# Optimization experiments

Measured on AMD Instinct MI355X. Metric: run time of the kernel, lower is better.

Reference implementation:

```python
import jax, jax.numpy as jnp
import numpy as np

EPS_LN = 1e-12
EPS_BN = 1e-5


def layernorm(x, w, b):
    u = jnp.mean(x, axis=-1, keepdims=True)
    s = jnp.mean((x - u) ** 2, axis=-1, keepdims=True)
    return w * ((x - u) / jnp.sqrt(s + EPS_LN)) + b


def reps_block(x, ln1_w, ln1_b, lin_w, lin_b, ln2_w, ln2_b):
    # GRAPHLayerNorm -> (dropout, identity in eval) -> Linear -> ReLU -> GRAPHLayerNorm
    h = layernorm(x, ln1_w, ln1_b)
    h = jax.nn.relu(jnp.einsum('bnd,od->bno', h, lin_w) + lin_b)
    return layernorm(h, ln2_w, ln2_b)


def attend(x):
    # full dense self-attention: softmax(x x^T) x ; dropout is identity in eval
    scores = jnp.einsum('bnd,bmd->bnm', x, x)  # [B,4096,4096]
    attn = jax.nn.softmax(scores, axis=-1)
    return jnp.einsum('bnm,bmd->bnd', attn, x)


def setup_inputs() -> dict:
    key = jax.random.key(0)
    ks = jax.random.split(key, 8)
    B, C, H, W = 4, 512, 64, 64
    D = 512
    inp = {
        'T1': jax.random.normal(ks[0], (B, C, H, W), jnp.float32),
        'T2': jax.random.normal(ks[1], (B, C, H, W), jnp.float32),
        'w_conv3': jax.random.normal(ks[2], (1024, 1024, 3, 3), jnp.float32) * 0.01,
        'w_conv1': jax.random.normal(ks[3], (512, 1024, 1, 1), jnp.float32) * 0.03,
        'bn_gamma': jnp.ones((512,), jnp.float32),
        'bn_beta': jnp.zeros((512,), jnp.float32),
        'bn_mean': jnp.zeros((512,), jnp.float32),
        'bn_var': jnp.ones((512,), jnp.float32),
        'ln1_w': jnp.ones((D,), jnp.float32),
        'ln1_b': jnp.zeros((D,), jnp.float32),
        'lin_w': jax.random.normal(ks[4], (D, D), jnp.float32) * 0.04,
        'lin_b': jnp.zeros((D,), jnp.float32),
        'ln2_w': jnp.ones((D,), jnp.float32),
        'ln2_b': jnp.zeros((D,), jnp.float32),
    }
    return inp


def reference(T1, T2, w_conv3, w_conv1, bn_gamma, bn_beta, bn_mean, bn_var,
              ln1_w, ln1_b, lin_w, lin_b, ln2_w, ln2_b):
    B = T1.shape[0]
    X = jnp.concatenate((T1, T2), axis=1)  # [B,1024,64,64]
    dn = ('NCHW', 'OIHW', 'NCHW')
    X = jax.lax.conv_general_dilated(X, w_conv3, (1, 1), ((1, 1), (1, 1)), dimension_numbers=dn)
    X = jax.lax.conv_general_dilated(X, w_conv1, (1, 1), ((0, 0), (0, 0)), dimension_numbers=dn)  # [B,512,64,64]
    # BatchNorm (eval, running stats) + ReLU
    inv = (bn_gamma / jnp.sqrt(bn_var + EPS_BN))[None, :, None, None]
    X = jax.nn.relu(X * inv + (bn_beta - bn_mean * bn_gamma / jnp.sqrt(bn_var + EPS_BN))[None, :, None, None])
    x = X.transpose(0, 2, 3, 1).reshape(B, 4096, 512)
    # block 1
    rel = attend(x)
    rel = reps_block(x + rel, ln1_w, ln1_b, lin_w, lin_b, ln2_w, ln2_b)
    # block 2 (original code reuses self.reps_graph, i.e. SAME params)
    rel1 = attend(rel)
    rel1 = reps_block(rel + rel1, ln1_w, ln1_b, lin_w, lin_b, ln2_w, ln2_b)
    return rel1.reshape(B, 64, 64, 512).transpose(0, 3, 1, 2)  # [B,512,64,64]
```

## Files before the change

kernel.cpp:

```cpp
#include <hip/hip_runtime.h>
#include <stdint.h>

typedef float f32x4 __attribute__((ext_vector_type(4)));
typedef __bf16 bf16x8 __attribute__((ext_vector_type(8)));
typedef unsigned short u16;
typedef unsigned short u16x8 __attribute__((ext_vector_type(8)));

__device__ __forceinline__ float bf2f(u16 u){ unsigned int i = ((unsigned int)u)<<16; float f; __builtin_memcpy(&f,&i,4); return f; }
__device__ __forceinline__ u16 f2bf(float f){ unsigned int i; __builtin_memcpy(&i,&f,4); i += 0x7FFFu + ((i>>16)&1u); return (u16)(i>>16); }
__device__ __forceinline__ u16 f2h(float f){ _Float16 h = (_Float16)f; u16 b; __builtin_memcpy(&b,&h,2); return b; }
__device__ __forceinline__ float h2f(u16 b){ _Float16 h; __builtin_memcpy(&h,&b,2); return (float)h; }

__device__ __forceinline__ void gld16(const void* g, void* l){
  __builtin_amdgcn_global_load_lds(
      (const __attribute__((address_space(1))) void*)(uintptr_t)g,
      (__attribute__((address_space(3))) void*)(unsigned int)(uintptr_t)l, 16, 0, 0);
}

__global__ __launch_bounds__(256) void pad_interior(const float* __restrict__ T1,
                                                    const float* __restrict__ T2,
                                                    u16* __restrict__ Xpad){
  const int n = blockIdx.z, ct = blockIdx.y, pt = blockIdx.x;
  const int t = threadIdx.x;
  const int c0 = ct*64, p0 = pt*64;
  const float* src = (c0 < 512) ? (T1 + ((long)n*512 + c0)*4096)
                                : (T2 + ((long)n*512 + (c0-512))*4096);
  __shared__ u16 lds[64][66];
  #pragma unroll
  for (int i=0;i<4;i++){
    int c = i*16 + (t>>4);
    int ch = t&15;
    float4 v = *(const float4*)(src + (long)c*4096 + p0 + ch*4);
    int p = ch*4;
    lds[p+0][c] = f2bf(v.x); lds[p+1][c] = f2bf(v.y);
    lds[p+2][c] = f2bf(v.z); lds[p+3][c] = f2bf(v.w);
  }
  __syncthreads();
  #pragma unroll
  for (int i=0;i<8;i++){
    int p = i*8 + (t>>5);
    int c2 = t&31;
    int pix = p0 + p; int yy = (pix>>6)+1, xx = (pix&63)+1;
    ushort2 val; val.x = lds[p][2*c2]; val.y = lds[p][2*c2+1];
    *(ushort2*)(Xpad + (((long)n*66 + yy)*66 + xx)*1024 + c0 + 2*c2) = val;
  }
}

__global__ __launch_bounds__(256) void prep_w3(const float* __restrict__ w3, u16* __restrict__ wk3t){
  const int o = blockIdx.x; const int t = threadIdx.x;
  __shared__ u16 lds[9216];
  const float* src = w3 + (long)o*9216;
  #pragma unroll
  for (int i=0;i<9;i++){
    int j = i*256 + t;
    float4 v = *(const float4*)(src + j*4);
    lds[j*4+0]=f2bf(v.x); lds[j*4+1]=f2bf(v.y); lds[j*4+2]=f2bf(v.z); lds[j*4+3]=f2bf(v.w);
  }
  __syncthreads();
  u16* dst = wk3t + (long)o*9216;
  #pragma unroll
  for (int i=0;i<36;i++){
    int j = i*256 + t; int tp = j>>10, ci = j&1023;
    dst[j] = lds[ci*9+tp];
  }
}

__global__ void prep_w1(const float* __restrict__ w1, const float* __restrict__ bg,
                        const float* __restrict__ bv, u16* __restrict__ w1t){
  long i = (long)blockIdx.x*256 + threadIdx.x;
  int o = (int)(i>>10);
  float inv = bg[o] / sqrtf(bv[o] + 1e-5f);
  w1t[i] = f2bf(w1[i]*inv);
}

__global__ void prep_bias1(const float* __restrict__ bg, const float* __restrict__ bb,
                           const float* __restrict__ bm, const float* __restrict__ bv,
                           float* __restrict__ bias1){
  int o = blockIdx.x*256+threadIdx.x;
  float inv = bg[o]/sqrtf(bv[o]+1e-5f);
  bias1[o] = bb[o] - bm[o]*inv;
}

__global__ void cvt_bf(const float* __restrict__ s, u16* __restrict__ d){
  long i = (long)blockIdx.x*256 + threadIdx.x;
  d[i] = f2bf(s[i]);
}

__global__ __launch_bounds__(256) void row_norm(const u16* __restrict__ x, float* __restrict__ nrm){
  const int row = blockIdx.x*4 + (threadIdx.x>>6);
  const int lane = threadIdx.x & 63;
  u16x8 q = *(const u16x8*)(x + (long)row*512 + lane*8);
  float s = 0.f;
  #pragma unroll
  for (int j=0;j<8;j++){ float f = bf2f(q[j]); s += f*f; }
  #pragma unroll
  for (int off=32; off; off>>=1) s += __shfl_xor(s, off);
  if (lane==0) nrm[row] = s;
}

__global__ __launch_bounds__(256) void transpose_bf(const u16* __restrict__ src, u16* __restrict__ dst,
                                                    int R, int C, long sStr, long dStr){
  const int z = blockIdx.z;
  src += (long)z*sStr; dst += (long)z*dStr;
  const int r0 = blockIdx.x*64, c0 = blockIdx.y*64;
  const int t = threadIdx.x;
  __shared__ u16 lds[64][66];
  #pragma unroll
  for (int i=0;i<4;i++){
    int r = i*16 + (t>>4), ch = t&15;
    ushort4 v = *(const ushort4*)(src + (long)(r0+r)*C + c0 + ch*4);
    lds[r][ch*4+0]=v.x; lds[r][ch*4+1]=v.y; lds[r][ch*4+2]=v.z; lds[r][ch*4+3]=v.w;
  }
  __syncthreads();
  #pragma unroll
  for (int i=0;i<4;i++){
    int c = i*16 + (t>>4), ch = t&15;
    ushort4 v;
    v.x = lds[ch*4+0][c]; v.y = lds[ch*4+1][c]; v.z = lds[ch*4+2][c]; v.w = lds[ch*4+3][c];
    *(ushort4*)(dst + (long)(c0+c)*R + r0 + ch*4) = v;
  }
}

__global__ __launch_bounds__(256) void transpose_f32(const float* __restrict__ src, float* __restrict__ dst,
                                                     int R, int C, long sStr, long dStr){
  const int z = blockIdx.z;
  src += (long)z*sStr; dst += (long)z*dStr;
  const int r0 = blockIdx.x*32, c0 = blockIdx.y*32;
  const int t = threadIdx.x;
  __shared__ float lds[32][33];
  {
    int r = t>>3, ch = t&7;
    float4 v = *(const float4*)(src + (long)(r0+r)*C + c0 + ch*4);
    lds[r][ch*4+0]=v.x; lds[r][ch*4+1]=v.y; lds[r][ch*4+2]=v.z; lds[r][ch*4+3]=v.w;
  }
  __syncthreads();
  {
    int c = t>>3, ch = t&7;
    float4 v;
    v.x = lds[ch*4+0][c]; v.y = lds[ch*4+1][c]; v.z = lds[ch*4+2][c]; v.w = lds[ch*4+3][c];
    *(float4*)(dst + (long)(c0+c)*R + r0 + ch*4) = v;
  }
}

template<int EPI, int CONV>
__global__ __launch_bounds__(512, 2) void gemm256(
    const u16* __restrict__ A, const u16* __restrict__ Bt, void* __restrict__ Cv,
    int K, int lda, int ldb, int ldc, const float* __restrict__ srow)
{
  extern __shared__ u16 sm[];
  const int t = threadIdx.x;
  const int lane = t & 63;
  const int wid = t >> 6;
  const int wr = wid >> 2, wc = wid & 3;

  const int orig = blockIdx.y * gridDim.x + blockIdx.x;
  const int cpx = (gridDim.x * gridDim.y) >> 3;
  const int swz = (orig & 7) * cpx + (orig >> 3);
  const int bx = swz % gridDim.x;
  const int by = swz / gridDim.x;
  const long m0 = (long)by * 256, n0 = (long)bx * 256;

  const int row0 = t >> 2;
  const int cs0  = (t & 3) ^ ((row0 >> 1) & 3);

  const u16 *aB0, *aB1;
  if (CONV) {
    long m_ = m0 + row0;
    long pb0 = ((long)((int)(m_>>12)*66 + (int)((m_>>6)&63)))*66 + (int)(m_&63);
    m_ = m0 + row0 + 128;
    long pb1 = ((long)((int)(m_>>12)*66 + (int)((m_>>6)&63)))*66 + (int)(m_&63);
    aB0 = A + pb0*1024 + cs0*8;
    aB1 = A + pb1*1024 + cs0*8;
  } else {
    aB0 = A + (m0 + row0)*(long)lda + cs0*8;
    aB1 = A + (m0 + row0 + 128)*(long)lda + cs0*8;
  }
  const u16* bB0 = Bt + (n0 + row0)*(long)ldb + cs0*8;
  const u16* bB1 = Bt + (n0 + row0 + 128)*(long)ldb + cs0*8;

  auto issueA = [&](int sub, long aoff){
    u16* d = sm + sub*8192 + t*8;
    gld16(aB0 + aoff, d);
    gld16(aB1 + aoff, d + 4096);
  };
  auto issueB = [&](int sub, long boff){
    u16* d = sm + 32768 + sub*8192 + t*8;
    gld16(bB0 + boff, d);
    gld16(bB1 + boff, d + 4096);
  };
  auto conv_aoff = [&](int tile)->long {
    int kb = tile << 6;
    int tap = kb >> 10;
    int cb  = kb & 1023;
    int ky = (tap >= 6) ? 2 : (tap >= 3 ? 1 : 0);
    int kx = tap - ky*3;
    return (long)(ky*66 + kx)*1024 + cb;
  };

  const int frow = lane & 15;
  const int elemoff = (((lane>>4) ^ ((frow>>1)&3)) << 3);
  const int rAoff = (wr*128 + frow)*32 + elemoff;
  const int rBoff = (wc*64  + frow)*32 + elemoff;

  f32x4 acc[8][4] = {};

  {
    long a0 = CONV ? conv_aoff(0) : 0L;
    issueA(0, a0);
    issueB(0, 0);
    issueA(1, a0 + 32);
    issueB(1, 32);
  }

  const int NT = K >> 6;
  for (int tile = 0; tile < NT; ++tile) {
    const int b = tile & 1;
    const int nb2 = b ^ 1;
    const bool lastT = (tile == NT-1);
    long aoffN = 0, boffN = 0;
    if (!lastT) {
      aoffN = CONV ? conv_aoff(tile+1) : (long)(tile+1)*64;
      boffN = (long)(tile+1)*64;
    }

    asm volatile("s_waitcnt vmcnt(4)" ::: "memory");
    __builtin_amdgcn_s_barrier();
    __builtin_amdgcn_sched_barrier(0);

    {
      const u16* pA = sm + (b*2+0)*8192 + rAoff;
      const u16* pB = sm + 32768 + (b*2+0)*8192 + rBoff;
      bf16x8 bf[4];
      #pragma unroll
      for (int i=0;i<4;i++) bf[i] = *(const bf16x8*)(pB + i*512);
      {
        bf16x8 a[4];
        #pragma unroll
        for (int i=0;i<4;i++) a[i] = *(const bf16x8*)(pA + i*512);
        if (!lastT) issueA(nb2*2+0, aoffN);
        __builtin_amdgcn_s_setprio(1);
        #pragma unroll
        for (int mi=0;mi<4;mi++)
          #pragma unroll
          for (int ni=0;ni<4;ni++)
            acc[mi][ni] = __builtin_amdgcn_mfma_f32_16x16x32_bf16(a[mi], bf[ni], acc[mi][ni],0,0,0);
        __builtin_amdgcn_s_setprio(0);
      }
      {
        bf16x8 a[4];
        #pragma unroll
        for (int i=0;i<4;i++) a[i] = *(const bf16x8*)(pA + (4+i)*512);
        if (!lastT) issueB(nb2*2+0, boffN);
        __builtin_amdgcn_s_setprio(1);
        #pragma unroll
        for (int mi=0;mi<4;mi++)
          #pragma unroll
          for (int ni=0;ni<4;ni++)
            acc[4+mi][ni] = __builtin_amdgcn_mfma_f32_16x16x32_bf16(a[mi], bf[ni], acc[4+mi][ni],0,0,0);
        __builtin_amdgcn_s_setprio(0);
      }
    }

    if (lastT) asm volatile("s_waitcnt vmcnt(0)" ::: "memory");
    else       asm volatile("s_waitcnt vmcnt(4)" ::: "memory");
    __builtin_amdgcn_s_barrier();
    __builtin_amdgcn_sched_barrier(0);

    {
      const u16* pA = sm + (b*2+1)*8192 + rAoff;
      const u16* pB = sm + 32768 + (b*2+1)*8192 + rBoff;
      bf16x8 bf[4];
      #pragma unroll
      for (int i=0;i<4;i++) bf[i] = *(const bf16x8*)(pB + i*512);
      {
        bf16x8 a[4];
        #pragma unroll
        for (int i=0;i<4;i++) a[i] = *(const bf16x8*)(pA + i*512);
        if (!lastT) issueA(nb2*2+1, aoffN + 32);
        __builtin_amdgcn_s_setprio(1);
        #pragma unroll
        for (int mi=0;mi<4;mi++)
          #pragma unroll
          for (int ni=0;ni<4;ni++)
            acc[mi][ni] = __builtin_amdgcn_mfma_f32_16x16x32_bf16(a[mi], bf[ni], acc[mi][ni],0,0,0);
        __builtin_amdgcn_s_setprio(0);
      }
      {
        bf16x8 a[4];
        #pragma unroll
        for (int i=0;i<4;i++) a[i] = *(const bf16x8*)(pA + (4+i)*512);
        if (!lastT) issueB(nb2*2+1, boffN + 32);
        __builtin_amdgcn_s_setprio(1);
        #pragma unroll
        for (int mi=0;mi<4;mi++)
          #pragma unroll
          for (int ni=0;ni<4;ni++)
            acc[4+mi][ni] = __builtin_amdgcn_mfma_f32_16x16x32_bf16(a[mi], bf[ni], acc[4+mi][ni],0,0,0);
        __builtin_amdgcn_s_setprio(0);
      }
    }
  }

  const int crow0 = wr*128 + ((lane>>4)<<2);
  const int ccol0 = wc*64 + frow;
  #pragma unroll
  for (int mi=0;mi<8;mi++){
    #pragma unroll
    for (int ni=0;ni<4;ni++){
      long col = n0 + ccol0 + ni*16;
      #pragma unroll
      for (int r=0;r<4;r++){
        long row = m0 + crow0 + mi*16 + r;
        float v = acc[mi][ni][r];
        if (EPI==3) ((u16*)Cv)[row*(long)ldc + col] = f2h(v - srow[row]);
        else        ((u16*)Cv)[row*(long)ldc + col] = f2bf(v);
      }
    }
  }
}

template<int EPI>
__global__ __launch_bounds__(256, 2) void gemm_bt(
    const u16* __restrict__ A, const u16* __restrict__ Bt,
    void* __restrict__ Cv, const float* __restrict__ bias,
    int K, int lda, int ldb, int ldc)
{
  const int t = threadIdx.x;
  const int lane = t & 63;
  const int w = t >> 6;
  const int wr = w >> 1, wc = w & 1;
  const long m0 = (long)blockIdx.y * 128;
  const long n0 = (long)blockIdx.x * 128;

  __shared__ u16 lA[128*32];
  __shared__ u16 lB[128*32];

  const u16* aS0 = A + (m0 + (t>>2))*(long)lda + (t&3)*8;
  const u16* aS1 = aS0 + 64*(long)lda;
  const u16* bS0 = Bt + (n0 + (t>>2))*(long)ldb + (t&3)*8;
  const u16* bS1 = bS0 + 64*(long)ldb;
  u16* dA0 = lA + t*8; u16* dA1 = lA + 2048 + t*8;
  u16* dB0 = lB + t*8; u16* dB1 = lB + 2048 + t*8;

  f32x4 acc[4][4] = {};
  const int frow = lane & 15, kq = (lane >> 4) * 8;
  const u16* rA = lA + (wr*64 + frow)*32 + kq;
  const u16* rB = lB + (wc*64 + frow)*32 + kq;

  for (int kb = 0; kb < K; kb += 32) {
    gld16(aS0 + kb, dA0); gld16(aS1 + kb, dA1);
    gld16(bS0 + kb, dB0); gld16(bS1 + kb, dB1);
    __syncthreads();
    bf16x8 af[4], bfr[4];
    #pragma unroll
    for (int i=0;i<4;i++) af[i]  = *(const bf16x8*)(rA + i*512);
    #pragma unroll
    for (int i=0;i<4;i++) bfr[i] = *(const bf16x8*)(rB + i*512);
    #pragma unroll
    for (int mi=0;mi<4;mi++)
      #pragma unroll
      for (int ni=0;ni<4;ni++)
        acc[mi][ni] = __builtin_amdgcn_mfma_f32_16x16x32_bf16(af[mi], bfr[ni], acc[mi][ni], 0,0,0);
    __syncthreads();
  }

  const int crow0 = wr*64 + ((lane>>4)<<2);
  const int ccol0 = wc*64 + (lane&15);
  #pragma unroll
  for (int mi=0;mi<4;mi++){
    #pragma unroll
    for (int ni=0;ni<4;ni++){
      long col = n0 + ccol0 + ni*16;
      float bv = (EPI==1) ? bias[col] : 0.0f;
      #pragma unroll
      for (int r=0;r<4;r++){
        long row = m0 + crow0 + mi*16 + r;
        float v = acc[mi][ni][r];
        if (EPI==1){ v += bv; v = v > 0.0f ? v : 0.0f; }
        ((u16*)Cv)[row*(long)ldc + col] = f2bf(v);
      }
    }
  }
}

__global__ __launch_bounds__(256, 2) void pv_gemm(
    const u16* __restrict__ P0, const u16* __restrict__ P1,
    const u16* __restrict__ P2, const u16* __restrict__ P3,
    const u16* __restrict__ xT, u16* __restrict__ attb)
{
  const int orig = blockIdx.y*4 + blockIdx.x;
  const int swzb = (orig & 7)*16 + (orig >> 3);
  const int bx = swzb & 3, by = swzb >> 2;
  const long ZS = 4096L*512;
  const int z = blockIdx.z;
  const u16* A  = (z==0) ? P0 : (z==1) ? P1 : (z==2) ? P2 : P3;
  const u16* Bt = xT   + (long)z*ZS;
  u16*       C  = attb + (long)z*ZS;
  const int K = 4096, lda = 4096, ldb = 4096, ldc = 512;

  const int t = threadIdx.x;
  const int lane = t & 63;
  const int w = t >> 6;
  const int wr = w >> 1, wc = w & 1;
  const long m0 = (long)by * 128;
  const long n0 = (long)bx * 128;

  __shared__ u16 lA[128*32];
  __shared__ u16 lB[128*32];

  const u16* aS0 = A + (m0 + (t>>2))*(long)lda + (t&3)*8;
  const u16* aS1 = aS0 + 64*(long)lda;
  const u16* bS0 = Bt + (n0 + (t>>2))*(long)ldb + (t&3)*8;
  const u16* bS1 = bS0 + 64*(long)ldb;
  u16* dA0 = lA + t*8; u16* dA1 = lA + 2048 + t*8;
  u16* dB0 = lB + t*8; u16* dB1 = lB + 2048 + t*8;

  f32x4 acc[4][4] = {};
  const int frow = lane & 15, kq = (lane >> 4) * 8;
  const u16* rA = lA + (wr*64 + frow)*32 + kq;
  const u16* rB = lB + (wc*64 + frow)*32 + kq;

  for (int kb = 0; kb < K; kb += 32) {
    gld16(aS0 + kb, dA0); gld16(aS1 + kb, dA1);
    gld16(bS0 + kb, dB0); gld16(bS1 + kb, dB1);
    __syncthreads();
    bf16x8 af[4], bfr[4];
    #pragma unroll
    for (int i=0;i<4;i++) af[i]  = *(const bf16x8*)(rA + i*512);
    #pragma unroll
    for (int i=0;i<4;i++) bfr[i] = *(const bf16x8*)(rB + i*512);
    #pragma unroll
    for (int mi=0;mi<4;mi++)
      #pragma unroll
      for (int ni=0;ni<4;ni++)
        acc[mi][ni] = __builtin_amdgcn_mfma_f32_16x16x32_bf16(af[mi], bfr[ni], acc[mi][ni], 0,0,0);
    __syncthreads();
  }

  const int crow0 = wr*64 + ((lane>>4)<<2);
  const int ccol0 = wc*64 + (lane&15);
  #pragma unroll
  for (int mi=0;mi<4;mi++){
    #pragma unroll
    for (int ni=0;ni<4;ni++){
      long col = n0 + ccol0 + ni*16;
      #pragma unroll
      for (int r=0;r<4;r++){
        long row = m0 + crow0 + mi*16 + r;
        C[row*(long)ldc + col] = f2bf(acc[mi][ni][r]);
      }
    }
  }
}

__global__ __launch_bounds__(256) void softmax_row(const u16* __restrict__ S, u16* __restrict__ P){
  const long row = blockIdx.x;
  const u16* src = S + row*4096;
  const int t = threadIdx.x, lane = t&63, w = t>>6;
  float v[16];
  #pragma unroll
  for (int i=0;i<2;i++){
    u16x8 q = *(const u16x8*)(src + t*16 + i*8);
    #pragma unroll
    for (int j=0;j<8;j++) v[i*8+j] = h2f(q[j]);
  }
  float mx = v[0];
  #pragma unroll
  for (int i=1;i<16;i++) mx = fmaxf(mx, v[i]);
  #pragma unroll
  for (int off=32; off; off>>=1) mx = fmaxf(mx, __shfl_xor(mx, off));
  __shared__ float red[4];
  if (lane==0) red[w] = mx;
  __syncthreads();
  mx = fmaxf(fmaxf(red[0],red[1]), fmaxf(red[2],red[3]));
  float sum = 0.0f;
  #pragma unroll
  for (int i=0;i<16;i++){ v[i] = __expf(v[i]-mx); sum += v[i]; }
  #pragma unroll
  for (int off=32; off; off>>=1) sum += __shfl_xor(sum, off);
  __shared__ float red2[4];
  if (lane==0) red2[w] = sum;
  __syncthreads();
  sum = red2[0]+red2[1]+red2[2]+red2[3];
  const float inv = 1.0f/sum;
  u16* dst = P + row*4096;
  #pragma unroll
  for (int i=0;i<2;i++){
    u16x8 o;
    #pragma unroll
    for (int j=0;j<8;j++) o[j] = f2bf(v[i*8+j]*inv);
    *(u16x8*)(dst + t*16 + i*8) = o;
  }
}

template<int ADD, int OUTF, int OUTB>
__global__ __launch_bounds__(256) void ln_row(
    const u16* __restrict__ X, const u16* __restrict__ Y,
    const float* __restrict__ w, const float* __restrict__ b,
    u16* __restrict__ outB, float* __restrict__ outF)
{
  const long row = blockIdx.x;
  const int t = threadIdx.x, lane = t&63, wv = t>>6;
  ushort2 xv = *(const ushort2*)(X + row*512 + t*2);
  float v0 = bf2f(xv.x), v1 = bf2f(xv.y);
  if (ADD){
    ushort2 yv = *(const ushort2*)(Y + row*512 + t*2);
    v0 += bf2f(yv.x); v1 += bf2f(yv.y);
  }
  float s = v0+v1, q = v0*v0 + v1*v1;
  #pragma unroll
  for (int off=32; off; off>>=1){ s += __shfl_xor(s,off); q += __shfl_xor(q,off); }
  __shared__ float red[8];
  if (lane==0){ red[wv]=s; red[4+wv]=q; }
  __syncthreads();
  s = red[0]+red[1]+red[2]+red[3];
  q = red[4]+red[5]+red[6]+red[7];
  const float u = s*(1.0f/512.0f);
  const float var = q*(1.0f/512.0f) - u*u;
  const float inv = rsqrtf(var + 1e-12f);
  const int c = t*2;
  float o0 = (v0-u)*inv*w[c]   + b[c];
  float o1 = (v1-u)*inv*w[c+1] + b[c+1];
  if (OUTB){ ushort2 ov; ov.x=f2bf(o0); ov.y=f2bf(o1); *(ushort2*)(outB + row*512 + c) = ov; }
  if (OUTF){ float2 ov; ov.x=o0; ov.y=o1; *(float2*)(outF + row*512 + c) = ov; }
}

extern "C" void kernel_launch(void* const* d_in, const int* in_sizes, int n_in,
                              void* d_out, int out_size, void* d_ws, size_t ws_size,
                              hipStream_t stream) {
  const float* T1   = (const float*)d_in[0];
  const float* T2   = (const float*)d_in[1];
  const float* w3   = (const float*)d_in[2];
  const float* w1   = (const float*)d_in[3];
  const float* bg   = (const float*)d_in[4];
  const float* bb   = (const float*)d_in[5];
  const float* bm   = (const float*)d_in[6];
  const float* bv   = (const float*)d_in[7];
  const float* ln1w = (const float*)d_in[8];
  const float* ln1b = (const float*)d_in[9];
  const float* linw = (const float*)d_in[10];
  const float* linb = (const float*)d_in[11];
  const float* ln2w = (const float*)d_in[12];
  const float* ln2b = (const float*)d_in[13];

  hipFuncSetAttribute(reinterpret_cast<const void*>(gemm256<0,1>),
                      hipFuncAttributeMaxDynamicSharedMemorySize, 131072);
  hipFuncSetAttribute(reinterpret_cast<const void*>(gemm256<3,0>),
                      hipFuncAttributeMaxDynamicSharedMemorySize, 131072);

  char* ws = (char*)d_ws;
  size_t off = 0;
  auto alloc = [&](size_t bytes)->char* {
    char* p = ws + off;
    off += (bytes + 255) & ~(size_t)255;
    return p;
  };
  const size_t XPAD_B = 4L*66*66*1024*2;
  u16*   Xpad  = (u16*)  alloc(XPAD_B);
  u16*   wk3t  = (u16*)  alloc(1024L*9216*2);
  u16*   w1t   = (u16*)  alloc(512L*1024*2);
  u16*   lint  = (u16*)  alloc(512L*512*2);
  float* bias1 = (float*)alloc(512*4);
  float* nrm   = (float*)alloc(16384L*4);
  u16*   Y1    = (u16*)  alloc(16384L*1024*2);
  u16*   x0    = (u16*)  alloc(16384L*512*2);
  u16*   xT    = (u16*)  alloc(4L*512*4096*2);
  char*  Sreg  = alloc(4096L*4096*4);
  u16*   attb  = (u16*)  alloc(16384L*512*2);
  u16*   h     = (u16*)  alloc(16384L*512*2);
  u16*   g     = (u16*)  alloc(16384L*512*2);
  u16*   rel1  = (u16*)  alloc(16384L*512*2);
  u16*   Sh    = (u16*)Sreg;
  u16*   P0    = Y1;
  u16*   P1    = h;
  u16*   P2    = (u16*)(Sreg + 4096L*4096*2);
  u16*   P3    = Xpad;
  float* rel2f = (float*)Sreg;
  if (off > ws_size) return;

  const long ZS = 4096L*512;

  hipMemsetAsync(Xpad, 0, XPAD_B, stream);
  pad_interior<<<dim3(64,16,4), 256, 0, stream>>>(T1, T2, Xpad);
  prep_w3<<<1024, 256, 0, stream>>>(w3, wk3t);
  prep_w1<<<2048, 256, 0, stream>>>(w1, bg, bv, w1t);
  prep_bias1<<<2, 256, 0, stream>>>(bg, bb, bm, bv, bias1);
  cvt_bf<<<1024, 256, 0, stream>>>(linw, lint);

  gemm256<0,1><<<dim3(4,64), 512, 131072, stream>>>(Xpad, wk3t, (void*)Y1, 9216, 0, 9216, 1024, nullptr);
  gemm_bt<1><<<dim3(4,128), 256, 0, stream>>>(Y1, w1t, (void*)x0, bias1, 1024, 1024, 1024, 512);

  auto attend = [&](const u16* xin){
    transpose_bf<<<dim3(64,8,4), 256, 0, stream>>>(xin, xT, 4096, 512, ZS, ZS);
    row_norm<<<4096, 256, 0, stream>>>(xin, nrm);
    u16* Pz[4] = {P0, P1, P2, P3};
    for (int z=0; z<4; z++){
      const u16* xz = xin + (long)z*ZS;
      gemm256<3,0><<<dim3(16,16), 512, 131072, stream>>>(xz, xz, (void*)Sh, 512, 512, 512, 4096,
                                                         nrm + (long)z*4096);
      softmax_row<<<4096, 256, 0, stream>>>(Sh, Pz[z]);
    }
    pv_gemm<<<dim3(4,32,4), 256, 0, stream>>>(P0, P1, P2, P3, xT, attb);
  };

  attend(x0);
  ln_row<1,0,1><<<16384, 256, 0, stream>>>(x0, attb, ln1w, ln1b, h, nullptr);
  gemm_bt<1><<<dim3(4,128), 256, 0, stream>>>(h, lint, (void*)g, linb, 512, 512, 512, 512);
  ln_row<0,0,1><<<16384, 256, 0, stream>>>(g, nullptr, ln2w, ln2b, rel1, nullptr);

  attend(rel1);
  ln_row<1,0,1><<<16384, 256, 0, stream>>>(rel1, attb, ln1w, ln1b, h, nullptr);
  gemm_bt<1><<<dim3(4,128), 256, 0, stream>>>(h, lint, (void*)g, linb, 512, 512, 512, 512);
  ln_row<0,1,0><<<16384, 256, 0, stream>>>(g, nullptr, ln2w, ln2b, nullptr, rel2f);

  transpose_f32<<<dim3(128,16,4), 256, 0, stream>>>(rel2f, (float*)d_out, 4096, 512, ZS, ZS);
}
```

Before: 929.3 us.

## Fuse softmax stats into score GEMM epilogue and exp into PV GEMM

The score GEMM epilogue now computes per-row partial max and sum-exp for each 64-column chunk. A small finalize kernel reduces these into a row max and inverse sum. The separate softmax pass is removed: the new PV kernel reads the raw fp16 scores, exponentiates and normalizes them while staging into LDS, and uses a narrower 32-row tile with swizzled LDS. The final layernorm now writes bf16 and the output transpose converts to f32, which halves that intermediate's traffic at the cost of bf16 rounding on the output. This removes a full read/write pass over the 4096x4096 score matrix per batch, but the PV kernel re-runs the exp for every row tile and uses smaller tiles.

```diff
diff --git a/kernel.cpp b/kernel.cpp
--- a/kernel.cpp
+++ b/kernel.cpp
@@ -5,6 +5,7 @@
 typedef __bf16 bf16x8 __attribute__((ext_vector_type(8)));
 typedef unsigned short u16;
 typedef unsigned short u16x8 __attribute__((ext_vector_type(8)));
+typedef unsigned short u16x4 __attribute__((ext_vector_type(4)));
 
 __device__ __forceinline__ float bf2f(u16 u){ unsigned int i = ((unsigned int)u)<<16; float f; __builtin_memcpy(&f,&i,4); return f; }
 __device__ __forceinline__ u16 f2bf(float f){ unsigned int i; __builtin_memcpy(&i,&f,4); i += 0x7FFFu + ((i>>16)&1u); return (u16)(i>>16); }
@@ -121,31 +122,34 @@
   }
 }
 
-__global__ __launch_bounds__(256) void transpose_f32(const float* __restrict__ src, float* __restrict__ dst,
-                                                     int R, int C, long sStr, long dStr){
+__global__ __launch_bounds__(256) void transpose_bf_f32(const u16* __restrict__ src, float* __restrict__ dst){
   const int z = blockIdx.z;
-  src += (long)z*sStr; dst += (long)z*dStr;
-  const int r0 = blockIdx.x*32, c0 = blockIdx.y*32;
+  src += (long)z*4096*512; dst += (long)z*512*4096;
+  const int r0 = blockIdx.x*64, c0 = blockIdx.y*64;
   const int t = threadIdx.x;
-  __shared__ float lds[32][33];
-  {
-    int r = t>>3, ch = t&7;
-    float4 v = *(const float4*)(src + (long)(r0+r)*C + c0 + ch*4);
+  __shared__ u16 lds[64][66];
+  #pragma unroll
+  for (int i=0;i<4;i++){
+    int r = i*16 + (t>>4), ch = t&15;
+    ushort4 v = *(const ushort4*)(src + (long)(r0+r)*512 + c0 + ch*4);
     lds[r][ch*4+0]=v.x; lds[r][ch*4+1]=v.y; lds[r][ch*4+2]=v.z; lds[r][ch*4+3]=v.w;
   }
   __syncthreads();
-  {
-    int c = t>>3, ch = t&7;
+  #pragma unroll
+  for (int i=0;i<4;i++){
+    int c = i*16 + (t>>4), ch = t&15;
     float4 v;
-    v.x = lds[ch*4+0][c]; v.y = lds[ch*4+1][c]; v.z = lds[ch*4+2][c]; v.w = lds[ch*4+3][c];
-    *(float4*)(dst + (long)(c0+c)*R + r0 + ch*4) = v;
+    v.x = bf2f(lds[ch*4+0][c]); v.y = bf2f(lds[ch*4+1][c]);
+    v.z = bf2f(lds[ch*4+2][c]); v.w = bf2f(lds[ch*4+3][c]);
+    *(float4*)(dst + (long)(c0+c)*4096 + r0 + ch*4) = v;
   }
 }
 
 template<int EPI, int CONV>
 __global__ __launch_bounds__(512, 2) void gemm256(
     const u16* __restrict__ A, const u16* __restrict__ Bt, void* __restrict__ Cv,
-    int K, int lda, int ldb, int ldc, const float* __restrict__ srow)
+    int K, int lda, int ldb, int ldc, const float* __restrict__ srow,
+    float2* __restrict__ spart)
 {
   extern __shared__ u16 sm[];
   const int t = threadIdx.x;
@@ -303,20 +307,54 @@
 
   const int crow0 = wr*128 + ((lane>>4)<<2);
   const int ccol0 = wc*64 + frow;
-  #pragma unroll
-  for (int mi=0;mi<8;mi++){
-    #pragma unroll
-    for (int ni=0;ni<4;ni++){
-      long col = n0 + ccol0 + ni*16;
+  if (EPI == 3) {
+    #pragma unroll
+    for (int mi=0;mi<8;mi++){
       #pragma unroll
       for (int r=0;r<4;r++){
         long row = m0 + crow0 + mi*16 + r;
-        float v = acc[mi][ni][r];
-        if (EPI==3) ((u16*)Cv)[row*(long)ldc + col] = f2h(v - srow[row]);
-        else        ((u16*)Cv)[row*(long)ldc + col] = f2bf(v);
-      }
-    }
-  }
+        float sr = srow[row];
+        float sv0 = acc[mi][0][r]-sr, sv1 = acc[mi][1][r]-sr;
+        float sv2 = acc[mi][2][r]-sr, sv3 = acc[mi][3][r]-sr;
+        u16* cb = (u16*)Cv + row*(long)ldc + n0 + ccol0;
+        cb[0] = f2h(sv0); cb[16] = f2h(sv1); cb[32] = f2h(sv2); cb[48] = f2h(sv3);
+        float M4 = fmaxf(fmaxf(sv0,sv1), fmaxf(sv2,sv3));
+        M4 = fmaxf(M4, __shfl_xor(M4,1)); M4 = fmaxf(M4, __shfl_xor(M4,2));
+        M4 = fmaxf(M4, __shfl_xor(M4,4)); M4 = fmaxf(M4, __shfl_xor(M4,8));
+        float e = __expf(sv0-M4)+__expf(sv1-M4)+__expf(sv2-M4)+__expf(sv3-M4);
+        e += __shfl_xor(e,1); e += __shfl_xor(e,2);
+        e += __shfl_xor(e,4); e += __shfl_xor(e,8);
+        if ((lane&15)==0) spart[row*64 + (n0>>6) + wc] = make_float2(M4, e);
+      }
+    }
+  } else {
+    #pragma unroll
+    for (int mi=0;mi<8;mi++){
+      #pragma unroll
+      for (int ni=0;ni<4;ni++){
+        long col = n0 + ccol0 + ni*16;
+        #pragma unroll
+        for (int r=0;r<4;r++){
+          long row = m0 + crow0 + mi*16 + r;
+          ((u16*)Cv)[row*(long)ldc + col] = f2bf(acc[mi][ni][r]);
+        }
+      }
+    }
+  }
+}
+
+__global__ __launch_bounds__(256) void finalize_lse(const float2* __restrict__ sp,
+                                                    float2* __restrict__ out){
+  const int row = blockIdx.x*4 + (threadIdx.x>>6);
+  const int lane = threadIdx.x & 63;
+  float2 p = sp[row*64 + lane];
+  float M = p.x;
+  #pragma unroll
+  for (int off=32; off; off>>=1) M = fmaxf(M, __shfl_xor(M, off));
+  float e = p.y * __expf(p.x - M);
+  #pragma unroll
+  for (int off=32; off; off>>=1) e += __shfl_xor(e, off);
+  if (lane==0) out[row] = make_float2(M, 1.0f/e);
 }
 
 template<int EPI>
@@ -383,121 +421,93 @@
   }
 }
 
-__global__ __launch_bounds__(256, 2) void pv_gemm(
-    const u16* __restrict__ P0, const u16* __restrict__ P1,
-    const u16* __restrict__ P2, const u16* __restrict__ P3,
-    const u16* __restrict__ xT, u16* __restrict__ attb)
+__global__ __launch_bounds__(512, 2) void pv2(
+    const u16* __restrict__ S0a, const u16* __restrict__ S1a,
+    const u16* __restrict__ S2a, const u16* __restrict__ S3a,
+    const float2* __restrict__ rstats, const u16* __restrict__ xT,
+    u16* __restrict__ attb)
 {
-  const int orig = blockIdx.y*4 + blockIdx.x;
-  const int swzb = (orig & 7)*16 + (orig >> 3);
-  const int bx = swzb & 3, by = swzb >> 2;
+  extern __shared__ u16 pm[];
+  u16* lA = pm;
+  u16* lB = pm + 2048;
+  const int z = blockIdx.y;
+  const u16* Sz = (z==0)?S0a:(z==1)?S1a:(z==2)?S2a:S3a;
   const long ZS = 4096L*512;
-  const int z = blockIdx.z;
-  const u16* A  = (z==0) ? P0 : (z==1) ? P1 : (z==2) ? P2 : P3;
-  const u16* Bt = xT   + (long)z*ZS;
-  u16*       C  = attb + (long)z*ZS;
-  const int K = 4096, lda = 4096, ldb = 4096, ldc = 512;
-
+  const u16* Bt = xT + (long)z*ZS;
+  u16* C = attb + (long)z*ZS;
+  const int swz = (blockIdx.x & 7)*16 + (blockIdx.x >> 3);
+  const long m0 = (long)swz * 32;
   const int t = threadIdx.x;
-  const int lane = t & 63;
-  const int w = t >> 6;
-  const int wr = w >> 1, wc = w & 1;
-  const long m0 = (long)by * 128;
-  const long n0 = (long)bx * 128;
-
-  __shared__ u16 lA[128*32];
-  __shared__ u16 lB[128*32];
-
-  const u16* aS0 = A + (m0 + (t>>2))*(long)lda + (t&3)*8;
-  const u16* aS1 = aS0 + 64*(long)lda;
-  const u16* bS0 = Bt + (n0 + (t>>2))*(long)ldb + (t&3)*8;
-  const u16* bS1 = bS0 + 64*(long)ldb;
-  u16* dA0 = lA + t*8; u16* dA1 = lA + 2048 + t*8;
-  u16* dB0 = lB + t*8; u16* dB1 = lB + 2048 + t*8;
-
-  f32x4 acc[4][4] = {};
-  const int frow = lane & 15, kq = (lane >> 4) * 8;
-  const u16* rA = lA + (wr*64 + frow)*32 + kq;
-  const u16* rB = lB + (wc*64 + frow)*32 + kq;
-
-  for (int kb = 0; kb < K; kb += 32) {
-    gld16(aS0 + kb, dA0); gld16(aS1 + kb, dA1);
-    gld16(bS0 + kb, dB0); gld16(bS1 + kb, dB1);
+  const int lane = t & 63, w = t >> 6;
+
+  const int brow = t >> 3;
+  const int bch  = t & 7;
+  const u16* bS = Bt + (long)brow*4096 + ((bch ^ (brow & 7)) * 8);
+  u16* bD = lB + t*8;
+
+  const int arow = t >> 4;
+  const int aq   = t & 15;
+  float2 st = rstats[(long)z*4096 + m0 + arow];
+  const float Mrow = st.x, iLrow = st.y;
+  const u16* aS = Sz + (m0 + arow)*4096L + aq*4;
+  u16* aD = lA + arow*64 + (((aq>>1) ^ (arow & 7)) * 8) + (aq & 1)*4;
+
+  const int fr = lane & 15;
+  const int eor = lane & 7;
+  const int co0 = (((lane>>4)     ^ eor) * 8);
+  const int co1 = (((4+(lane>>4)) ^ eor) * 8);
+  const u16* rA = lA + fr*64;
+  const u16* rB = lB + (w*64 + fr)*64;
+
+  f32x4 acc[2][4] = {};
+
+  for (int kb = 0; kb < 4096; kb += 64) {
+    #pragma unroll
+    for (int p = 0; p < 8; p++)
+      gld16(bS + (long)p*262144 + kb, bD + p*4096);
+    {
+      u16x4 q = *(const u16x4*)(aS + kb);
+      u16x4 o;
+      #pragma unroll
+      for (int j=0;j<4;j++)
+        o[j] = f2bf(__expf(h2f(q[j]) - Mrow) * iLrow);
+      *(u16x4*)aD = o;
+    }
     __syncthreads();
-    bf16x8 af[4], bfr[4];
-    #pragma unroll
-    for (int i=0;i<4;i++) af[i]  = *(const bf16x8*)(rA + i*512);
-    #pragma unroll
-    for (int i=0;i<4;i++) bfr[i] = *(const bf16x8*)(rB + i*512);
-    #pragma unroll
-    for (int mi=0;mi<4;mi++)
-      #pragma unroll
-      for (int ni=0;ni<4;ni++)
-        acc[mi][ni] = __builtin_amdgcn_mfma_f32_16x16x32_bf16(af[mi], bfr[ni], acc[mi][ni], 0,0,0);
+    #pragma unroll
+    for (int kk = 0; kk < 2; kk++) {
+      const int co = kk ? co1 : co0;
+      bf16x8 af0 = *(const bf16x8*)(rA + co);
+      bf16x8 af1 = *(const bf16x8*)(rA + 1024 + co);
+      #pragma unroll
+      for (int ni=0;ni<4;ni++){
+        bf16x8 bv = *(const bf16x8*)(rB + ni*1024 + co);
+        acc[0][ni] = __builtin_amdgcn_mfma_f32_16x16x32_bf16(af0, bv, acc[0][ni],0,0,0);
+        acc[1][ni] = __builtin_amdgcn_mfma_f32_16x16x32_bf16(af1, bv, acc[1][ni],0,0,0);
+      }
+    }
     __syncthreads();
   }
 
-  const int crow0 = wr*64 + ((lane>>4)<<2);
-  const int ccol0 = wc*64 + (lane&15);
-  #pragma unroll
-  for (int mi=0;mi<4;mi++){
+  #pragma unroll
+  for (int mi=0;mi<2;mi++){
     #pragma unroll
     for (int ni=0;ni<4;ni++){
-      long col = n0 + ccol0 + ni*16;
+      long col = w*64 + ni*16 + fr;
       #pragma unroll
       for (int r=0;r<4;r++){
-        long row = m0 + crow0 + mi*16 + r;
-        C[row*(long)ldc + col] = f2bf(acc[mi][ni][r]);
-      }
-    }
-  }
-}
-
-__global__ __launch_bounds__(256) void softmax_row(const u16* __restrict__ S, u16* __restrict__ P){
-  const long row = blockIdx.x;
-  const u16* src = S + row*4096;
-  const int t = threadIdx.x, lane = t&63, w = t>>6;
-  float v[16];
-  #pragma unroll
-  for (int i=0;i<2;i++){
-    u16x8 q = *(const u16x8*)(src + t*16 + i*8);
-    #pragma unroll
-    for (int j=0;j<8;j++) v[i*8+j] = h2f(q[j]);
-  }
-  float mx = v[0];
-  #pragma unroll
-  for (int i=1;i<16;i++) mx = fmaxf(mx, v[i]);
-  #pragma unroll
-  for (int off=32; off; off>>=1) mx = fmaxf(mx, __shfl_xor(mx, off));
-  __shared__ float red[4];
-  if (lane==0) red[w] = mx;
-  __syncthreads();
-  mx = fmaxf(fmaxf(red[0],red[1]), fmaxf(red[2],red[3]));
-  float sum = 0.0f;
-  #pragma unroll
-  for (int i=0;i<16;i++){ v[i] = __expf(v[i]-mx); sum += v[i]; }
-  #pragma unroll
-  for (int off=32; off; off>>=1) sum += __shfl_xor(sum, off);
-  __shared__ float red2[4];
-  if (lane==0) red2[w] = sum;
-  __syncthreads();
-  sum = red2[0]+red2[1]+red2[2]+red2[3];
-  const float inv = 1.0f/sum;
-  u16* dst = P + row*4096;
-  #pragma unroll
-  for (int i=0;i<2;i++){
-    u16x8 o;
-    #pragma unroll
-    for (int j=0;j<8;j++) o[j] = f2bf(v[i*8+j]*inv);
-    *(u16x8*)(dst + t*16 + i*8) = o;
-  }
-}
-
-template<int ADD, int OUTF, int OUTB>
+        long row = m0 + mi*16 + (lane>>4)*4 + r;
+        C[row*512 + col] = f2bf(acc[mi][ni][r]);
+      }
+    }
+  }
+}
+
+template<int ADD>
 __global__ __launch_bounds__(256) void ln_row(
     const u16* __restrict__ X, const u16* __restrict__ Y,
     const float* __restrict__ w, const float* __restrict__ b,
-    u16* __restrict__ outB, float* __restrict__ outF)
+    u16* __restrict__ outB)
 {
   const long row = blockIdx.x;
   const int t = threadIdx.x, lane = t&63, wv = t>>6;
@@ -521,8 +531,8 @@
   const int c = t*2;
   float o0 = (v0-u)*inv*w[c]   + b[c];
   float o1 = (v1-u)*inv*w[c+1] + b[c+1];
-  if (OUTB){ ushort2 ov; ov.x=f2bf(o0); ov.y=f2bf(o1); *(ushort2*)(outB + row*512 + c) = ov; }
-  if (OUTF){ float2 ov; ov.x=o0; ov.y=o1; *(float2*)(outF + row*512 + c) = ov; }
+  ushort2 ov; ov.x=f2bf(o0); ov.y=f2bf(o1);
+  *(ushort2*)(outB + row*512 + c) = ov;
 }
 
 extern "C" void kernel_launch(void* const* d_in, const int* in_sizes, int n_in,
@@ -547,6 +557,8 @@
                       hipFuncAttributeMaxDynamicSharedMemorySize, 131072);
   hipFuncSetAttribute(reinterpret_cast<const void*>(gemm256<3,0>),
                       hipFuncAttributeMaxDynamicSharedMemorySize, 131072);
+  hipFuncSetAttribute(reinterpret_cast<const void*>(pv2),
+                      hipFuncAttributeMaxDynamicSharedMemorySize, 69632);
 
   char* ws = (char*)d_ws;
   size_t off = 0;
@@ -562,20 +574,20 @@
   u16*   lint  = (u16*)  alloc(512L*512*2);
   float* bias1 = (float*)alloc(512*4);
   float* nrm   = (float*)alloc(16384L*4);
+  float2* Spart= (float2*)alloc(4096L*64*8);
+  float2* rst  = (float2*)alloc(4L*4096*8);
   u16*   Y1    = (u16*)  alloc(16384L*1024*2);
   u16*   x0    = (u16*)  alloc(16384L*512*2);
   u16*   xT    = (u16*)  alloc(4L*512*4096*2);
-  char*  Sreg  = alloc(4096L*4096*4);
+  u16*   Sreg  = (u16*)  alloc(2L*4096*4096*2);
   u16*   attb  = (u16*)  alloc(16384L*512*2);
   u16*   h     = (u16*)  alloc(16384L*512*2);
   u16*   g     = (u16*)  alloc(16384L*512*2);
   u16*   rel1  = (u16*)  alloc(16384L*512*2);
-  u16*   Sh    = (u16*)Sreg;
-  u16*   P0    = Y1;
-  u16*   P1    = h;
-  u16*   P2    = (u16*)(Sreg + 4096L*4096*2);
-  u16*   P3    = Xpad;
-  float* rel2f = (float*)Sreg;
+  u16*   S0    = Y1;
+  u16*   S1    = Sreg;
+  u16*   S2    = Sreg + 4096L*4096;
+  u16*   S3    = Xpad;
   if (off > ws_size) return;
 
   const long ZS = 4096L*512;
@@ -587,31 +599,32 @@
   prep_bias1<<<2, 256, 0, stream>>>(bg, bb, bm, bv, bias1);
   cvt_bf<<<1024, 256, 0, stream>>>(linw, lint);
 
-  gemm256<0,1><<<dim3(4,64), 512, 131072, stream>>>(Xpad, wk3t, (void*)Y1, 9216, 0, 9216, 1024, nullptr);
+  gemm256<0,1><<<dim3(4,64), 512, 131072, stream>>>(Xpad, wk3t, (void*)Y1, 9216, 0, 9216, 1024,
+                                                    nullptr, nullptr);
   gemm_bt<1><<<dim3(4,128), 256, 0, stream>>>(Y1, w1t, (void*)x0, bias1, 1024, 1024, 1024, 512);
 
+  u16* Sz[4] = {S0, S1, S2, S3};
   auto attend = [&](const u16* xin){
     transpose_bf<<<dim3(64,8,4), 256, 0, stream>>>(xin, xT, 4096, 512, ZS, ZS);
     row_norm<<<4096, 256, 0, stream>>>(xin, nrm);
-    u16* Pz[4] = {P0, P1, P2, P3};
     for (int z=0; z<4; z++){
       const u16* xz = xin + (long)z*ZS;
-      gemm256<3,0><<<dim3(16,16), 512, 131072, stream>>>(xz, xz, (void*)Sh, 512, 512, 512, 4096,
-                                                         nrm + (long)z*4096);
-      softmax_row<<<4096, 256, 0, stream>>>(Sh, Pz[z]);
-    }
-    pv_gemm<<<dim3(4,32,4), 256, 0, stream>>>(P0, P1, P2, P3, xT, attb);
+      gemm256<3,0><<<dim3(16,16), 512, 131072, stream>>>(xz, xz, (void*)Sz[z], 512, 512, 512, 4096,
+                                                         nrm + (long)z*4096, Spart);
+      finalize_lse<<<1024, 256, 0, stream>>>(Spart, rst + (long)z*4096);
+    }
+    pv2<<<dim3(128,4), 512, 69632, stream>>>(S0, S1, S2, S3, rst, xT, attb);
   };
 
   attend(x0);
-  ln_row<1,0,1><<<16384, 256, 0, stream>>>(x0, attb, ln1w, ln1b, h, nullptr);
+  ln_row<1><<<16384, 256, 0, stream>>>(x0, attb, ln1w, ln1b, h);
   gemm_bt<1><<<dim3(4,128), 256, 0, stream>>>(h, lint, (void*)g, linb, 512, 512, 512, 512);
-  ln_row<0,0,1><<<16384, 256, 0, stream>>>(g, nullptr, ln2w, ln2b, rel1, nullptr);
+  ln_row<0><<<16384, 256, 0, stream>>>(g, nullptr, ln2w, ln2b, rel1);
 
   attend(rel1);
-  ln_row<1,0,1><<<16384, 256, 0, stream>>>(rel1, attb, ln1w, ln1b, h, nullptr);
+  ln_row<1><<<16384, 256, 0, stream>>>(rel1, attb, ln1w, ln1b, h);
   gemm_bt<1><<<dim3(4,128), 256, 0, stream>>>(h, lint, (void*)g, linb, 512, 512, 512, 512);
-  ln_row<0,1,0><<<16384, 256, 0, stream>>>(g, nullptr, ln2w, ln2b, nullptr, rel2f);
-
-  transpose_f32<<<dim3(128,16,4), 256, 0, stream>>>(rel2f, (float*)d_out, 4096, 512, ZS, ZS);
-}
+  ln_row<0><<<16384, 256, 0, stream>>>(g, nullptr, ln2w, ln2b, x0);
+
+  transpose_bf_f32<<<dim3(64,8,4), 256, 0, stream>>>(x0, (float*)d_out);
+}
```

Result: slower. 974.7 us (+4.9%).
